# Performance work log

Measured on AMD Instinct MI355X. Metric: run time of the kernel, lower is better.

Reference implementation:

```python
import jax, jax.numpy as jnp
import numpy as np

H = 16
D = 72
SCALE = D ** -0.5

def rotate_half(x):
    x1, x2 = jnp.split(x, 2, axis=-1)
    return jnp.concatenate([-x2, x1], axis=-1)

def setup_inputs() -> dict:
    key = jax.random.key(0)
    ks = jax.random.split(key, 7)
    S, E = 4096, 1152
    hidden_states = jax.random.normal(ks[0], (S, E), dtype=jnp.float32)
    cos = jax.random.uniform(ks[1], (S, D), dtype=jnp.float32)
    sin = jax.random.uniform(ks[2], (S, D), dtype=jnp.float32)
    qkv_w = jax.random.normal(ks[3], (3 * E, E), dtype=jnp.float32) * (E ** -0.5)
    qkv_b = jax.random.normal(ks[4], (3 * E,), dtype=jnp.float32) * 0.02
    proj_w = jax.random.normal(ks[5], (E, E), dtype=jnp.float32) * (E ** -0.5)
    proj_b = jax.random.normal(ks[6], (E,), dtype=jnp.float32) * 0.02
    cu_seqlens = jnp.arange(5, dtype=jnp.int32) * (S // 4)  # 4 equal image chunks
    return {"hidden_states": hidden_states, "cos": cos, "sin": sin,
            "qkv_w": qkv_w, "qkv_b": qkv_b, "proj_w": proj_w, "proj_b": proj_b,
            "cu_seqlens": cu_seqlens}

def reference(hidden_states, cos, sin, qkv_w, qkv_b, proj_w, proj_b, cu_seqlens):
    S, E = hidden_states.shape
    n_chunks = cu_seqlens.shape[0] - 1  # static; equal-length chunks assumed
    L = S // n_chunks
    # QKV projection
    qkv = hidden_states @ qkv_w.T + qkv_b            # (S, 3E)
    qkv = qkv.reshape(S, 3, H, D)
    q, k, v = qkv[:, 0], qkv[:, 1], qkv[:, 2]        # each (S, H, D)
    # RoPE in fp32 (inputs are fp32 already)
    c = cos[:, None, :].astype(jnp.float32)
    s = sin[:, None, :].astype(jnp.float32)
    qf, kf = q.astype(jnp.float32), k.astype(jnp.float32)
    q = (qf * c + rotate_half(qf) * s).astype(q.dtype)
    k = (kf * c + rotate_half(kf) * s).astype(k.dtype)
    # Batched varlen attention: reshape equal chunks to a batch axis
    qb = q.reshape(n_chunks, L, H, D)
    kb = k.reshape(n_chunks, L, H, D)
    vb = v.reshape(n_chunks, L, H, D)
    scores = jnp.einsum('blhd,bmhd->bhlm', qb, kb) * SCALE
    probs = jax.nn.softmax(scores.astype(jnp.float32), axis=-1).astype(q.dtype)
    attn = jnp.einsum('bhlm,bmhd->blhd', probs, vb)  # (nc, L, H, D)
    attn = attn.reshape(S, H * D)
    return attn @ proj_w.T + proj_b
```

## Files before the change

### kernel.cpp

```cpp
#include <hip/hip_runtime.h>
#include <hip/hip_bf16.h>


#define S_TOT 4096
#define E_DIM 1152
#define QKV_N 3456
#define NH    16
#define HD    72
#define HDP   96
#define CLEN  1024

static constexpr float SCALE_QK = 0.11785113019775793f;

typedef __bf16 bf16x8 __attribute__((ext_vector_type(8)));
typedef float  f32x4  __attribute__((ext_vector_type(4)));
typedef __hip_bfloat16 bf16;

__device__ __forceinline__ void gld_lds16(const void* g, void* l) {
  __builtin_amdgcn_global_load_lds(
      (const __attribute__((address_space(1))) unsigned int*)g,
      (__attribute__((address_space(3))) unsigned int*)l, 16, 0, 0);
}

__device__ __forceinline__ void stage128x32(const bf16* src, int ld, bf16* dst,
                                            int w, int ln) {
#pragma unroll
  for (int c = 0; c < 2; ++c) {
    const int f = ((w * 2 + c) * 64 + ln) * 8;
    gld_lds16(src + (f >> 5) * ld + (f & 31), dst + (w * 2 + c) * 512);
  }
}

__device__ __forceinline__ void stage128x96(const bf16* src, bf16* dst,
                                            int w, int ln) {
#pragma unroll
  for (int j = 0; j < 6; ++j) {
    const int f = (w * 6 + j) * 64 + ln;
    const int row = f / 12, c = f % 12;
    gld_lds16(src + row * 96 + ((c ^ (row & 3)) << 3), dst + f * 8);
  }
}

__device__ __forceinline__ void stageVt(const bf16* src, bf16* dst,
                                        int w, int ln) {
#pragma unroll
  for (int j = 0; j < 6; ++j) {
    const int f = (w * 6 + j) * 64 + ln;
    const int d = f >> 4, c = f & 15;
    gld_lds16(src + (size_t)d * S_TOT + ((c ^ (d & 7)) << 3), dst + f * 8);
  }
}

__global__ void k_pack_plain(const float* __restrict__ x, bf16* __restrict__ y) {
  const int i = blockIdx.x * blockDim.x + threadIdx.x;
  const float4 v = ((const float4*)x)[i];
  y[4 * i + 0] = __float2bfloat16(v.x);
  y[4 * i + 1] = __float2bfloat16(v.y);
  y[4 * i + 2] = __float2bfloat16(v.z);
  y[4 * i + 3] = __float2bfloat16(v.w);
}

__global__ __launch_bounds__(256, 2)
void k_qkv_gemm(const bf16* __restrict__ Ab, const bf16* __restrict__ Wb,
                const float* __restrict__ bias, bf16* __restrict__ C) {
  __shared__ bf16 sA[128 * 32], sB[128 * 32];
  const int w = threadIdx.x >> 6, ln = threadIdx.x & 63;
  const int m0 = blockIdx.x * 128, n0 = blockIdx.y * 128;
  const bf16* A = Ab + (size_t)m0 * E_DIM;
  const bf16* B = Wb + (size_t)n0 * E_DIM;
  const int r = ln & 15, g = ln >> 4;
  const int wr = (w >> 1) * 64, wc = (w & 1) * 64;
  f32x4 acc[4][4] = {};
  for (int k0 = 0; k0 < E_DIM; k0 += 32) {
    __syncthreads();
    stage128x32(A + k0, E_DIM, sA, w, ln);
    stage128x32(B + k0, E_DIM, sB, w, ln);
    __syncthreads();
    bf16x8 a[4];
#pragma unroll
    for (int m = 0; m < 4; ++m)
      a[m] = *(const bf16x8*)&sA[(wr + m * 16 + r) * 32 + g * 8];
#pragma unroll
    for (int n = 0; n < 4; ++n) {
      bf16x8 bv = *(const bf16x8*)&sB[(wc + n * 16 + r) * 32 + g * 8];
#pragma unroll
      for (int m = 0; m < 4; ++m)
        acc[m][n] = __builtin_amdgcn_mfma_f32_16x16x32_bf16(a[m], bv, acc[m][n], 0, 0, 0);
    }
  }
#pragma unroll
  for (int n = 0; n < 4; ++n) {
    const int col = n0 + wc + n * 16 + r;
    const float bv = bias[col];
#pragma unroll
    for (int m = 0; m < 4; ++m)
#pragma unroll
      for (int j = 0; j < 4; ++j) {
        const int row = m0 + wr + m * 16 + g * 4 + j;
        C[(size_t)row * QKV_N + col] = __float2bfloat16(acc[m][n][j] + bv);
      }
  }
}

__global__ void k_vtrans(const bf16* __restrict__ Qkv, bf16* __restrict__ Vt) {
  __shared__ bf16 t[32][33];
  const int hd0 = blockIdx.x * 32, s0 = blockIdx.y * 32;
  const int tx = threadIdx.x, ty = threadIdx.y;
#pragma unroll
  for (int k = 0; k < 4; ++k)
    t[ty + 8 * k][tx] = Qkv[(size_t)(s0 + ty + 8 * k) * QKV_N + 2304 + hd0 + tx];
  __syncthreads();
#pragma unroll
  for (int k = 0; k < 4; ++k) {
    const int hd = hd0 + ty + 8 * k;
    const int hh = hd / HD, dd = hd % HD;
    Vt[((size_t)hh * HDP + dd) * S_TOT + s0 + tx] = t[tx][ty + 8 * k];
  }
}

__global__ void k_rope(const bf16* __restrict__ Qkv,
                       const float* __restrict__ cs, const float* __restrict__ sn,
                       bf16* __restrict__ Qh, bf16* __restrict__ Kh) {
  const int i = blockIdx.x * 256 + threadIdx.x;
  const int d = i % 48;
  const int h = (i / 48) & 15;
  const int s = i / (48 * 16);
  const size_t ob = ((size_t)h * S_TOT + s) * HDP;
  if (d >= 36) {
    const int z = d - 36;
    const bf16 zero = __float2bfloat16(0.f);
    Qh[ob + 72 + z] = zero; Qh[ob + 84 + z] = zero;
    Kh[ob + 72 + z] = zero; Kh[ob + 84 + z] = zero;
    return;
  }
  const float c0 = cs[s * HD + d], s0 = sn[s * HD + d];
  const float c1 = cs[s * HD + d + 36], s1 = sn[s * HD + d + 36];
  const size_t qi = (size_t)s * QKV_N + h * HD;
  {
    const float x0 = __bfloat162float(Qkv[qi + d]);
    const float x1 = __bfloat162float(Qkv[qi + d + 36]);
    Qh[ob + d]      = __float2bfloat16((x0 * c0 - x1 * s0) * SCALE_QK);
    Qh[ob + d + 36] = __float2bfloat16((x1 * c1 + x0 * s1) * SCALE_QK);
  }
  {
    const float x0 = __bfloat162float(Qkv[qi + 1152 + d]);
    const float x1 = __bfloat162float(Qkv[qi + 1152 + d + 36]);
    Kh[ob + d]      = __float2bfloat16(x0 * c0 - x1 * s0);
    Kh[ob + d + 36] = __float2bfloat16(x1 * c1 + x0 * s1);
  }
}

__global__ __launch_bounds__(256, 2)
void k_flash(const bf16* __restrict__ Qh, const bf16* __restrict__ Kh,
             const bf16* __restrict__ Vt, bf16* __restrict__ Jb) {
  __shared__ bf16 sK[128 * 96];
  __shared__ bf16 sV[96 * 128];
  __shared__ bf16 sP[4 * 4096];
  const int w = threadIdx.x >> 6, ln = threadIdx.x & 63;
  const int r = ln & 15, g = ln >> 4;
  const int h = blockIdx.y, s0 = blockIdx.z * CLEN;
  const int q0 = blockIdx.x * 128;
  const bf16* Qg = Qh + ((size_t)h * S_TOT + s0 + q0) * HDP;
  const bf16* Kg = Kh + ((size_t)h * S_TOT + s0) * HDP;
  const bf16* Vg = Vt + (size_t)h * HDP * S_TOT + s0;

  stage128x96(Qg, sP, w, ln);
  __syncthreads();
  const char* sPb = (const char*)sP;
  bf16x8 qa[2][3];
#pragma unroll
  for (int m = 0; m < 2; ++m)
#pragma unroll
    for (int ks = 0; ks < 3; ++ks) {
      const int row = w * 32 + m * 16 + r;
      qa[m][ks] = *(const bf16x8*)(sPb + row * 192 + (((ks * 4 + g) ^ (row & 3)) << 4));
    }

  f32x4 oacc[2][6] = {};
  float mrun[2][4], lrun[2][4];
#pragma unroll
  for (int m = 0; m < 2; ++m)
#pragma unroll
    for (int j = 0; j < 4; ++j) { mrun[m][j] = -1e30f; lrun[m][j] = 0.f; }

  char* sPw = (char*)sP + w * 8192;
  const char* sKb = (const char*)sK;
  const char* sVb = (const char*)sV;

  for (int t = 0; t < 8; ++t) {
    __syncthreads();
    stage128x96(Kg + t * 128 * HDP, sK, w, ln);
    stageVt(Vg + t * 128, sV, w, ln);
    __syncthreads();

    f32x4 acc[2][8] = {};
#pragma unroll
    for (int ks = 0; ks < 3; ++ks)
#pragma unroll
      for (int n = 0; n < 8; ++n) {
        const int kv = n * 16 + r;
        bf16x8 bv = *(const bf16x8*)(sKb + kv * 192 + (((ks * 4 + g) ^ (kv & 3)) << 4));
        acc[0][n] = __builtin_amdgcn_mfma_f32_16x16x32_bf16(qa[0][ks], bv, acc[0][n], 0, 0, 0);
        acc[1][n] = __builtin_amdgcn_mfma_f32_16x16x32_bf16(qa[1][ks], bv, acc[1][n], 0, 0, 0);
      }

#pragma unroll
    for (int m = 0; m < 2; ++m)
#pragma unroll
      for (int j = 0; j < 4; ++j) {
        float tm = acc[m][0][j];
#pragma unroll
        for (int n = 1; n < 8; ++n) tm = fmaxf(tm, acc[m][n][j]);
#pragma unroll
        for (int o = 1; o < 16; o <<= 1) tm = fmaxf(tm, __shfl_xor(tm, o));
        const float mn = fmaxf(mrun[m][j], tm);
        const float esc = __expf(mrun[m][j] - mn);
        mrun[m][j] = mn;
        float sm = 0.f;
#pragma unroll
        for (int n = 0; n < 8; ++n) {
          const float p = __expf(acc[m][n][j] - mn);
          acc[m][n][j] = p; sm += p;
        }
#pragma unroll
        for (int o = 1; o < 16; o <<= 1) sm += __shfl_xor(sm, o);
        lrun[m][j] = lrun[m][j] * esc + sm;
#pragma unroll
        for (int n = 0; n < 6; ++n) oacc[m][n][j] *= esc;
      }

#pragma unroll
    for (int m = 0; m < 2; ++m)
#pragma unroll
      for (int n = 0; n < 8; ++n) {
        const int kv = n * 16 + r;
        const int gr = kv >> 3, wi = kv & 7;
#pragma unroll
        for (int j = 0; j < 4; ++j) {
          const int q = g * 4 + j;
          *(bf16*)(sPw + m * 4096 + q * 256 + ((gr ^ (q & 7)) << 4) + wi * 2) =
              __float2bfloat16(acc[m][n][j]);
        }
      }

#pragma unroll
    for (int ks = 0; ks < 4; ++ks) {
      bf16x8 pa[2];
#pragma unroll
      for (int m = 0; m < 2; ++m)
        pa[m] = *(const bf16x8*)(sPw + m * 4096 + r * 256 +
                                 (((ks * 4 + g) ^ (r & 7)) << 4));
#pragma unroll
      for (int n = 0; n < 6; ++n) {
        const int d = n * 16 + r;
        bf16x8 vb = *(const bf16x8*)(sVb + d * 256 + (((ks * 4 + g) ^ (d & 7)) << 4));
        oacc[0][n] = __builtin_amdgcn_mfma_f32_16x16x32_bf16(pa[0], vb, oacc[0][n], 0, 0, 0);
        oacc[1][n] = __builtin_amdgcn_mfma_f32_16x16x32_bf16(pa[1], vb, oacc[1][n], 0, 0, 0);
      }
    }
  }

#pragma unroll
  for (int m = 0; m < 2; ++m) {
    float inv[4];
#pragma unroll
    for (int j = 0; j < 4; ++j) inv[j] = 1.0f / lrun[m][j];
#pragma unroll
    for (int n = 0; n < 6; ++n) {
      const int d = n * 16 + r;
      if (d < HD) {
#pragma unroll
        for (int j = 0; j < 4; ++j) {
          const int row = s0 + q0 + w * 32 + m * 16 + g * 4 + j;
          Jb[(size_t)row * E_DIM + h * HD + d] = __float2bfloat16(oacc[m][n][j] * inv[j]);
        }
      }
    }
  }
}

__global__ __launch_bounds__(256, 2)
void k_proj(const bf16* __restrict__ Jb, const bf16* __restrict__ Pw,
            const float* __restrict__ bias, float* __restrict__ out) {
  __shared__ bf16 sA[128 * 32], sB[128 * 32];
  const int w = threadIdx.x >> 6, ln = threadIdx.x & 63;
  const int m0 = blockIdx.x * 128, n0 = blockIdx.y * 128;
  const bf16* A = Jb + (size_t)m0 * E_DIM;
  const bf16* B = Pw + (size_t)n0 * E_DIM;
  const int r = ln & 15, g = ln >> 4;
  const int wr = (w >> 1) * 64, wc = (w & 1) * 64;
  f32x4 acc[4][4] = {};
  for (int k0 = 0; k0 < E_DIM; k0 += 32) {
    __syncthreads();
    stage128x32(A + k0, E_DIM, sA, w, ln);
    stage128x32(B + k0, E_DIM, sB, w, ln);
    __syncthreads();
    bf16x8 a[4];
#pragma unroll
    for (int m = 0; m < 4; ++m)
      a[m] = *(const bf16x8*)&sA[(wr + m * 16 + r) * 32 + g * 8];
#pragma unroll
    for (int n = 0; n < 4; ++n) {
      bf16x8 bv = *(const bf16x8*)&sB[(wc + n * 16 + r) * 32 + g * 8];
#pragma unroll
      for (int m = 0; m < 4; ++m)
        acc[m][n] = __builtin_amdgcn_mfma_f32_16x16x32_bf16(a[m], bv, acc[m][n], 0, 0, 0);
    }
  }
#pragma unroll
  for (int n = 0; n < 4; ++n) {
    const int col = n0 + wc + n * 16 + r;
    const float bv = bias[col];
#pragma unroll
    for (int m = 0; m < 4; ++m)
#pragma unroll
      for (int j = 0; j < 4; ++j) {
        const int row = m0 + wr + m * 16 + g * 4 + j;
        out[(size_t)row * E_DIM + col] = acc[m][n][j] + bv;
      }
  }
}

extern "C" void kernel_launch(void* const* d_in, const int* in_sizes, int n_in,
                              void* d_out, int out_size, void* d_ws, size_t ws_size,
                              hipStream_t stream) {
  (void)in_sizes; (void)n_in; (void)out_size; (void)ws_size;
  const float* hs   = (const float*)d_in[0];
  const float* cosp = (const float*)d_in[1];
  const float* sinp = (const float*)d_in[2];
  const float* qkvw = (const float*)d_in[3];
  const float* qkvb = (const float*)d_in[4];
  const float* pw   = (const float*)d_in[5];
  const float* pb   = (const float*)d_in[6];
  float* out = (float*)d_out;
  char* ws = (char*)d_ws;

  bf16* Ab   = (bf16*)(ws + 0);
  bf16* Wb   = (bf16*)(ws + 9437184);
  bf16* Pw   = (bf16*)(ws + 17399808);
  bf16* Qkv  = (bf16*)(ws + 20054016);
  bf16* Qh   = (bf16*)(ws + 48365568);
  bf16* Kh   = (bf16*)(ws + 60948480);
  bf16* Vt   = (bf16*)(ws + 73531392);
  bf16* Jb   = (bf16*)(ws + 86114304);

  hipMemsetAsync(ws + 73531392, 0, 12582912, stream);

  k_pack_plain<<<4608, 256, 0, stream>>>(hs, Ab);
  k_pack_plain<<<3888, 256, 0, stream>>>(qkvw, Wb);
  k_pack_plain<<<1296, 256, 0, stream>>>(pw, Pw);
  k_qkv_gemm<<<dim3(32, 27), 256, 0, stream>>>(Ab, Wb, qkvb, Qkv);
  k_vtrans<<<dim3(36, 128), dim3(32, 8), 0, stream>>>(Qkv, Vt);
  k_rope<<<12288, 256, 0, stream>>>(Qkv, cosp, sinp, Qh, Kh);
  k_flash<<<dim3(8, 16, 4), 256, 0, stream>>>(Qh, Kh, Vt, Jb);
  k_proj<<<dim3(32, 9), 256, 0, stream>>>(Jb, Pw, pb, out);
}
```

Measured before the change: 249.6 us.

## Restructure flash kernel: transposed S=K·Q MFMA, trimmed V tiles, split waits

The flash attention kernel now computes the score tile transposed (K as the A operand), so each lane holds one query row's values and the softmax max and sum need only two cross-lane shuffles instead of four per row. P is written to LDS as packed 64-bit stores instead of single bf16 stores. The V staging and the PV MFMA loop drop from 6 to 5 16-wide d-blocks, since 72 columns fit in 80. A partial vmcnt wait lets the QK matmul start before the V loads finish, and the grid is reordered so head/chunk is the fastest-varying block index. This adds hand-written waitcnt and barrier logic that depends on the exact count of issued loads.

After: 237.5 us. 4.8% less time.

```diff
diff --git a/kernel.cpp b/kernel.cpp
--- a/kernel.cpp
+++ b/kernel.cpp
@@ -14,6 +14,7 @@
 
 typedef __bf16 bf16x8 __attribute__((ext_vector_type(8)));
 typedef float  f32x4  __attribute__((ext_vector_type(4)));
+typedef unsigned int u32x2 __attribute__((ext_vector_type(2)));
 typedef __hip_bfloat16 bf16;
 
 __device__ __forceinline__ void gld_lds16(const void* g, void* l) {
@@ -41,14 +42,20 @@
   }
 }
 
-__device__ __forceinline__ void stageVt(const bf16* src, bf16* dst,
-                                        int w, int ln) {
-#pragma unroll
-  for (int j = 0; j < 6; ++j) {
-    const int f = (w * 6 + j) * 64 + ln;
+__device__ __forceinline__ void stageVt5(const bf16* src, bf16* dst,
+                                         int w, int ln) {
+#pragma unroll
+  for (int j = 0; j < 5; ++j) {
+    const int f = (w * 5 + j) * 64 + ln;
     const int d = f >> 4, c = f & 15;
     gld_lds16(src + (size_t)d * S_TOT + ((c ^ (d & 7)) << 3), dst + f * 8);
   }
+}
+
+__device__ __forceinline__ unsigned pack2(float a, float b) {
+  const unsigned ua = __builtin_bit_cast(unsigned short, __float2bfloat16(a));
+  const unsigned ub = __builtin_bit_cast(unsigned short, __float2bfloat16(b));
+  return ua | (ub << 16);
 }
 
 __global__ void k_pack_plain(const float* __restrict__ x, bf16* __restrict__ y) {
@@ -158,8 +165,9 @@
   __shared__ bf16 sP[4 * 4096];
   const int w = threadIdx.x >> 6, ln = threadIdx.x & 63;
   const int r = ln & 15, g = ln >> 4;
-  const int h = blockIdx.y, s0 = blockIdx.z * CLEN;
-  const int q0 = blockIdx.x * 128;
+  const int hc = blockIdx.x;
+  const int h = hc >> 2, s0 = (hc & 3) * CLEN;
+  const int q0 = blockIdx.y * 128;
   const bf16* Qg = Qh + ((size_t)h * S_TOT + s0 + q0) * HDP;
   const bf16* Kg = Kh + ((size_t)h * S_TOT + s0) * HDP;
   const bf16* Vg = Vt + (size_t)h * HDP * S_TOT + s0;
@@ -176,72 +184,83 @@
       qa[m][ks] = *(const bf16x8*)(sPb + row * 192 + (((ks * 4 + g) ^ (row & 3)) << 4));
     }
 
-  f32x4 oacc[2][6] = {};
-  float mrun[2][4], lrun[2][4];
-#pragma unroll
-  for (int m = 0; m < 2; ++m)
-#pragma unroll
-    for (int j = 0; j < 4; ++j) { mrun[m][j] = -1e30f; lrun[m][j] = 0.f; }
+  f32x4 oacc[2][5] = {};
+  float mrun[2] = {-1e30f, -1e30f}, lrun[2] = {0.f, 0.f};
 
   char* sPw = (char*)sP + w * 8192;
   const char* sKb = (const char*)sK;
   const char* sVb = (const char*)sV;
+  const int ksw = r & 3;
 
   for (int t = 0; t < 8; ++t) {
     __syncthreads();
     stage128x96(Kg + t * 128 * HDP, sK, w, ln);
-    stageVt(Vg + t * 128, sV, w, ln);
-    __syncthreads();
+    stageVt5(Vg + t * 128, sV, w, ln);
+    asm volatile("s_waitcnt vmcnt(5)" ::: "memory");
+    __builtin_amdgcn_s_barrier();
 
     f32x4 acc[2][8] = {};
 #pragma unroll
-    for (int ks = 0; ks < 3; ++ks)
-#pragma unroll
-      for (int n = 0; n < 8; ++n) {
-        const int kv = n * 16 + r;
-        bf16x8 bv = *(const bf16x8*)(sKb + kv * 192 + (((ks * 4 + g) ^ (kv & 3)) << 4));
-        acc[0][n] = __builtin_amdgcn_mfma_f32_16x16x32_bf16(qa[0][ks], bv, acc[0][n], 0, 0, 0);
-        acc[1][n] = __builtin_amdgcn_mfma_f32_16x16x32_bf16(qa[1][ks], bv, acc[1][n], 0, 0, 0);
-      }
-
+    for (int kvb = 0; kvb < 8; ++kvb) {
+      bf16x8 ka[3];
+      const int row = kvb * 16 + r;
+#pragma unroll
+      for (int ks = 0; ks < 3; ++ks)
+        ka[ks] = *(const bf16x8*)(sKb + row * 192 + (((ks * 4 + g) ^ ksw) << 4));
+#pragma unroll
+      for (int ks = 0; ks < 3; ++ks) {
+        acc[0][kvb] = __builtin_amdgcn_mfma_f32_16x16x32_bf16(ka[ks], qa[0][ks], acc[0][kvb], 0, 0, 0);
+        acc[1][kvb] = __builtin_amdgcn_mfma_f32_16x16x32_bf16(ka[ks], qa[1][ks], acc[1][kvb], 0, 0, 0);
+      }
+    }
+
+    float escr[2];
+#pragma unroll
+    for (int m = 0; m < 2; ++m) {
+      float tm = acc[m][0][0];
+#pragma unroll
+      for (int kvb = 0; kvb < 8; ++kvb)
+#pragma unroll
+        for (int j = 0; j < 4; ++j) tm = fmaxf(tm, acc[m][kvb][j]);
+      tm = fmaxf(tm, __shfl_xor(tm, 16));
+      tm = fmaxf(tm, __shfl_xor(tm, 32));
+      const float mn = fmaxf(mrun[m], tm);
+      escr[m] = __expf(mrun[m] - mn);
+      mrun[m] = mn;
+      float sm = 0.f;
+#pragma unroll
+      for (int kvb = 0; kvb < 8; ++kvb)
+#pragma unroll
+        for (int j = 0; j < 4; ++j) {
+          const float p = __expf(acc[m][kvb][j] - mn);
+          acc[m][kvb][j] = p; sm += p;
+        }
+      sm += __shfl_xor(sm, 16);
+      sm += __shfl_xor(sm, 32);
+      lrun[m] = lrun[m] * escr[m] + sm;
+    }
 #pragma unroll
     for (int m = 0; m < 2; ++m)
 #pragma unroll
       for (int j = 0; j < 4; ++j) {
-        float tm = acc[m][0][j];
-#pragma unroll
-        for (int n = 1; n < 8; ++n) tm = fmaxf(tm, acc[m][n][j]);
-#pragma unroll
-        for (int o = 1; o < 16; o <<= 1) tm = fmaxf(tm, __shfl_xor(tm, o));
-        const float mn = fmaxf(mrun[m][j], tm);
-        const float esc = __expf(mrun[m][j] - mn);
-        mrun[m][j] = mn;
-        float sm = 0.f;
-#pragma unroll
-        for (int n = 0; n < 8; ++n) {
-          const float p = __expf(acc[m][n][j] - mn);
-          acc[m][n][j] = p; sm += p;
-        }
-#pragma unroll
-        for (int o = 1; o < 16; o <<= 1) sm += __shfl_xor(sm, o);
-        lrun[m][j] = lrun[m][j] * esc + sm;
-#pragma unroll
-        for (int n = 0; n < 6; ++n) oacc[m][n][j] *= esc;
+        const float e = __shfl(escr[m], (ln & 48) | (g * 4 + j));
+#pragma unroll
+        for (int n = 0; n < 5; ++n) oacc[m][n][j] *= e;
       }
 
 #pragma unroll
     for (int m = 0; m < 2; ++m)
 #pragma unroll
-      for (int n = 0; n < 8; ++n) {
-        const int kv = n * 16 + r;
-        const int gr = kv >> 3, wi = kv & 7;
-#pragma unroll
-        for (int j = 0; j < 4; ++j) {
-          const int q = g * 4 + j;
-          *(bf16*)(sPw + m * 4096 + q * 256 + ((gr ^ (q & 7)) << 4) + wi * 2) =
-              __float2bfloat16(acc[m][n][j]);
-        }
-      }
+      for (int kvb = 0; kvb < 8; ++kvb) {
+        u32x2 u;
+        u.x = pack2(acc[m][kvb][0], acc[m][kvb][1]);
+        u.y = pack2(acc[m][kvb][2], acc[m][kvb][3]);
+        const int gsw = (kvb * 2 + (g >> 1)) ^ (r & 7);
+        *(u32x2*)(sPw + m * 4096 + r * 256 + (gsw << 4) + (g & 1) * 8) = u;
+      }
+
+    asm volatile("s_waitcnt vmcnt(0)" ::: "memory");
+    __builtin_amdgcn_s_barrier();
 
 #pragma unroll
     for (int ks = 0; ks < 4; ++ks) {
@@ -251,7 +270,7 @@
         pa[m] = *(const bf16x8*)(sPw + m * 4096 + r * 256 +
                                  (((ks * 4 + g) ^ (r & 7)) << 4));
 #pragma unroll
-      for (int n = 0; n < 6; ++n) {
+      for (int n = 0; n < 5; ++n) {
         const int d = n * 16 + r;
         bf16x8 vb = *(const bf16x8*)(sVb + d * 256 + (((ks * 4 + g) ^ (d & 7)) << 4));
         oacc[0][n] = __builtin_amdgcn_mfma_f32_16x16x32_bf16(pa[0], vb, oacc[0][n], 0, 0, 0);
@@ -264,9 +283,10 @@
   for (int m = 0; m < 2; ++m) {
     float inv[4];
 #pragma unroll
-    for (int j = 0; j < 4; ++j) inv[j] = 1.0f / lrun[m][j];
-#pragma unroll
-    for (int n = 0; n < 6; ++n) {
+    for (int j = 0; j < 4; ++j)
+      inv[j] = 1.0f / __shfl(lrun[m], (ln & 48) | (g * 4 + j));
+#pragma unroll
+    for (int n = 0; n < 5; ++n) {
       const int d = n * 16 + r;
       if (d < HD) {
 #pragma unroll
@@ -352,6 +372,6 @@
   k_qkv_gemm<<<dim3(32, 27), 256, 0, stream>>>(Ab, Wb, qkvb, Qkv);
   k_vtrans<<<dim3(36, 128), dim3(32, 8), 0, stream>>>(Qkv, Vt);
   k_rope<<<12288, 256, 0, stream>>>(Qkv, cosp, sinp, Qh, Kh);
-  k_flash<<<dim3(8, 16, 4), 256, 0, stream>>>(Qh, Kh, Vt, Jb);
+  k_flash<<<dim3(64, 8), 256, 0, stream>>>(Qh, Kh, Vt, Jb);
   k_proj<<<dim3(32, 9), 256, 0, stream>>>(Jb, Pw, pb, out);
 }
```
